# Performance work log

Hardware: AMD Instinct MI355X
Metric: run time of the kernel (lower is better)

The kernel has to match this reference:

```python
import jax, jax.numpy as jnp
import numpy as np

# permutations for num_sources == 3 (matches task2perm[3])
PERMS3 = np.array([[0, 1, 2], [0, 2, 1], [1, 0, 2], [1, 2, 0], [2, 0, 1], [2, 1, 0]])
NUM_SOURCES = 3


def setup_inputs() -> dict:
    key = jax.random.key(0)
    k1, k2 = jax.random.split(key)
    shape = (16, 4096, NUM_SOURCES, 512)  # [bs, seq_len, num_sources, input_dim]
    return {
        "predictions": jax.random.normal(k1, shape, dtype=jnp.float32),
        "ground_truths": jax.random.normal(k2, shape, dtype=jnp.float32),
    }


def reference(predictions, ground_truths):
    n = NUM_SOURCES
    # Pairwise Frobenius distances over (seq_len, input_dim):
    # D[b, s_pred, s_gt] = ||preds[b,:,s_pred,:] - gts[b,:,s_gt,:]||_F
    # computed via ||a||^2 + ||b||^2 - 2<a,b> to avoid 6 permuted diff tensors.
    pn = jnp.sum(predictions * predictions, axis=(1, 3))        # [b, n]
    gn = jnp.sum(ground_truths * ground_truths, axis=(1, 3))    # [b, n]
    cross = jnp.einsum('btsd,btrd->bsr', predictions, ground_truths)  # [b, n, n]
    D = jnp.sqrt(jnp.maximum(pn[:, :, None] + gn[:, None, :] - 2.0 * cross, 0.0))

    perms = jnp.asarray(PERMS3)                                 # [P, n]
    # dists[b, p, s] = D[b, s, perms[p, s]]
    dists = D[:, jnp.arange(n)[None, :], perms]                 # [b, P, n]
    sum_ = jnp.sum(dists, axis=-1) / n                          # [b, P]
    # torch: sqrt(sum_**2).mean() == mean(|sum_|) over batch
    loss_per_perm = jnp.mean(jnp.abs(sum_), axis=0)             # [P]
    return jnp.log(jnp.min(loss_per_perm))
```

## Files before the change

### kernel.cpp

```cpp
#include <hip/hip_runtime.h>
#include <math.h>

#define B_DIM 16
#define T_DIM 4096
#define NSRC 3
#define D_DIM 512
#define DC_PER_ROW (D_DIM / 4)
#define BLOCKS_PER_B 128
#define T_PER_BLOCK (T_DIM / BLOCKS_PER_B)

__device__ __forceinline__ float dot4(float4 a, float4 b) {
    float r = a.x * b.x;
    r = fmaf(a.y, b.y, r);
    r = fmaf(a.z, b.z, r);
    r = fmaf(a.w, b.w, r);
    return r;
}

__global__ __launch_bounds__(256) void minloss_partial(
        const float* __restrict__ P, const float* __restrict__ G,
        float* __restrict__ ws) {
    const int bid   = blockIdx.x;
    const int b     = bid >> 7;
    const int chunk = bid & (BLOCKS_PER_B - 1);
    const int tid   = threadIdx.x;
    const int dc    = tid & (DC_PER_ROW - 1);
    const int tp    = tid >> 7;

    const size_t b_off = (size_t)b * T_DIM * NSRC * DC_PER_ROW;
    const float4* __restrict__ Pb = (const float4*)P + b_off;
    const float4* __restrict__ Gb = (const float4*)G + b_off;

    float acc[15];
#pragma unroll
    for (int k = 0; k < 15; ++k) acc[k] = 0.0f;

    const int t0 = chunk * T_PER_BLOCK;
    for (int t = t0 + tp; t < t0 + T_PER_BLOCK; t += 2) {
        const float4* __restrict__ Pr = Pb + (size_t)t * NSRC * DC_PER_ROW;
        const float4* __restrict__ Gr = Gb + (size_t)t * NSRC * DC_PER_ROW;
        float4 p0 = Pr[dc];
        float4 p1 = Pr[DC_PER_ROW + dc];
        float4 p2 = Pr[2 * DC_PER_ROW + dc];
        float4 g0 = Gr[dc];
        float4 g1 = Gr[DC_PER_ROW + dc];
        float4 g2 = Gr[2 * DC_PER_ROW + dc];

        acc[0] += dot4(p0, p0);
        acc[1] += dot4(p1, p1);
        acc[2] += dot4(p2, p2);
        acc[3] += dot4(g0, g0);
        acc[4] += dot4(g1, g1);
        acc[5] += dot4(g2, g2);
        acc[6]  += dot4(p0, g0);
        acc[7]  += dot4(p0, g1);
        acc[8]  += dot4(p0, g2);
        acc[9]  += dot4(p1, g0);
        acc[10] += dot4(p1, g1);
        acc[11] += dot4(p1, g2);
        acc[12] += dot4(p2, g0);
        acc[13] += dot4(p2, g1);
        acc[14] += dot4(p2, g2);
    }

#pragma unroll
    for (int k = 0; k < 15; ++k) {
        float v = acc[k];
#pragma unroll
        for (int off = 32; off > 0; off >>= 1)
            v += __shfl_down(v, off);
        acc[k] = v;
    }

    __shared__ float sm[4][15];
    const int wid  = tid >> 6;
    const int lane = tid & 63;
    if (lane == 0) {
#pragma unroll
        for (int k = 0; k < 15; ++k) sm[wid][k] = acc[k];
    }
    __syncthreads();
    if (tid < 15) {
        float v = sm[0][tid] + sm[1][tid] + sm[2][tid] + sm[3][tid];
        atomicAdd(&ws[b * 15 + tid], v);
    }
}

__global__ void minloss_finalize(const float* __restrict__ ws,
                                 float* __restrict__ out) {
    if (threadIdx.x != 0 || blockIdx.x != 0) return;
    const int perms[6][3] = {{0,1,2},{0,2,1},{1,0,2},{1,2,0},{2,0,1},{2,1,0}};
    float accp[6] = {0.f, 0.f, 0.f, 0.f, 0.f, 0.f};
    for (int b = 0; b < B_DIM; ++b) {
        const float* w = ws + b * 15;
        float D[3][3];
#pragma unroll
        for (int s = 0; s < 3; ++s)
#pragma unroll
            for (int r = 0; r < 3; ++r) {
                float v = w[s] + w[3 + r] - 2.0f * w[6 + s * 3 + r];
                D[s][r] = sqrtf(fmaxf(v, 0.0f));
            }
#pragma unroll
        for (int p = 0; p < 6; ++p) {
            float su = (D[0][perms[p][0]] + D[1][perms[p][1]] +
                        D[2][perms[p][2]]) * (1.0f / 3.0f);
            accp[p] += fabsf(su);
        }
    }
    float mn = 3.0e38f;
#pragma unroll
    for (int p = 0; p < 6; ++p) {
        float loss = accp[p] * (1.0f / (float)B_DIM);
        mn = fminf(mn, loss);
    }
    out[0] = logf(mn);
}

extern "C" void kernel_launch(void* const* d_in, const int* in_sizes, int n_in,
                              void* d_out, int out_size, void* d_ws, size_t ws_size,
                              hipStream_t stream) {
    const float* P = (const float*)d_in[0];
    const float* G = (const float*)d_in[1];
    float* out = (float*)d_out;
    float* ws  = (float*)d_ws;

    hipMemsetAsync(ws, 0, B_DIM * 15 * sizeof(float), stream);
    minloss_partial<<<B_DIM * BLOCKS_PER_B, 256, 0, stream>>>(P, G, ws);
    minloss_finalize<<<1, 64, 0, stream>>>(ws, out);
}
```

Before: 159.8 us.

## Unroll rows with nontemporal loads and replace atomics with per-block partials

Each loop iteration now loads two time rows using nontemporal vector loads, increasing loads in flight and hinting the cache to avoid retaining streamed data. The per-batch atomicAdd plus workspace memset is replaced by per-block partial writes that a wider finalize kernel reduces in shared memory. This removes a memset launch and atomic contention but adds a serial 128-element reduction per thread in finalize and changes the floating-point summation order.

```diff
diff --git a/kernel.cpp b/kernel.cpp
--- a/kernel.cpp
+++ b/kernel.cpp
@@ -9,7 +9,9 @@
 #define BLOCKS_PER_B 128
 #define T_PER_BLOCK (T_DIM / BLOCKS_PER_B)
 
-__device__ __forceinline__ float dot4(float4 a, float4 b) {
+typedef float f4 __attribute__((ext_vector_type(4)));
+
+__device__ __forceinline__ float dot4(f4 a, f4 b) {
     float r = a.x * b.x;
     r = fmaf(a.y, b.y, r);
     r = fmaf(a.z, b.z, r);
@@ -28,39 +30,48 @@
     const int tp    = tid >> 7;
 
     const size_t b_off = (size_t)b * T_DIM * NSRC * DC_PER_ROW;
-    const float4* __restrict__ Pb = (const float4*)P + b_off;
-    const float4* __restrict__ Gb = (const float4*)G + b_off;
+    const f4* __restrict__ Pb = (const f4*)P + b_off;
+    const f4* __restrict__ Gb = (const f4*)G + b_off;
 
     float acc[15];
 #pragma unroll
     for (int k = 0; k < 15; ++k) acc[k] = 0.0f;
 
     const int t0 = chunk * T_PER_BLOCK;
-    for (int t = t0 + tp; t < t0 + T_PER_BLOCK; t += 2) {
-        const float4* __restrict__ Pr = Pb + (size_t)t * NSRC * DC_PER_ROW;
-        const float4* __restrict__ Gr = Gb + (size_t)t * NSRC * DC_PER_ROW;
-        float4 p0 = Pr[dc];
-        float4 p1 = Pr[DC_PER_ROW + dc];
-        float4 p2 = Pr[2 * DC_PER_ROW + dc];
-        float4 g0 = Gr[dc];
-        float4 g1 = Gr[DC_PER_ROW + dc];
-        float4 g2 = Gr[2 * DC_PER_ROW + dc];
+    for (int t = t0 + tp; t < t0 + T_PER_BLOCK; t += 4) {
+        const f4* __restrict__ Pr0 = Pb + (size_t)t * NSRC * DC_PER_ROW;
+        const f4* __restrict__ Gr0 = Gb + (size_t)t * NSRC * DC_PER_ROW;
+        const f4* __restrict__ Pr1 = Pr0 + 2 * NSRC * DC_PER_ROW;
+        const f4* __restrict__ Gr1 = Gr0 + 2 * NSRC * DC_PER_ROW;
 
-        acc[0] += dot4(p0, p0);
-        acc[1] += dot4(p1, p1);
-        acc[2] += dot4(p2, p2);
-        acc[3] += dot4(g0, g0);
-        acc[4] += dot4(g1, g1);
-        acc[5] += dot4(g2, g2);
-        acc[6]  += dot4(p0, g0);
-        acc[7]  += dot4(p0, g1);
-        acc[8]  += dot4(p0, g2);
-        acc[9]  += dot4(p1, g0);
-        acc[10] += dot4(p1, g1);
-        acc[11] += dot4(p1, g2);
-        acc[12] += dot4(p2, g0);
-        acc[13] += dot4(p2, g1);
-        acc[14] += dot4(p2, g2);
+        f4 p0 = __builtin_nontemporal_load(Pr0 + dc);
+        f4 p1 = __builtin_nontemporal_load(Pr0 + DC_PER_ROW + dc);
+        f4 p2 = __builtin_nontemporal_load(Pr0 + 2 * DC_PER_ROW + dc);
+        f4 g0 = __builtin_nontemporal_load(Gr0 + dc);
+        f4 g1 = __builtin_nontemporal_load(Gr0 + DC_PER_ROW + dc);
+        f4 g2 = __builtin_nontemporal_load(Gr0 + 2 * DC_PER_ROW + dc);
+        f4 q0 = __builtin_nontemporal_load(Pr1 + dc);
+        f4 q1 = __builtin_nontemporal_load(Pr1 + DC_PER_ROW + dc);
+        f4 q2 = __builtin_nontemporal_load(Pr1 + 2 * DC_PER_ROW + dc);
+        f4 h0 = __builtin_nontemporal_load(Gr1 + dc);
+        f4 h1 = __builtin_nontemporal_load(Gr1 + DC_PER_ROW + dc);
+        f4 h2 = __builtin_nontemporal_load(Gr1 + 2 * DC_PER_ROW + dc);
+
+        acc[0] += dot4(p0, p0) + dot4(q0, q0);
+        acc[1] += dot4(p1, p1) + dot4(q1, q1);
+        acc[2] += dot4(p2, p2) + dot4(q2, q2);
+        acc[3] += dot4(g0, g0) + dot4(h0, h0);
+        acc[4] += dot4(g1, g1) + dot4(h1, h1);
+        acc[5] += dot4(g2, g2) + dot4(h2, h2);
+        acc[6]  += dot4(p0, g0) + dot4(q0, h0);
+        acc[7]  += dot4(p0, g1) + dot4(q0, h1);
+        acc[8]  += dot4(p0, g2) + dot4(q0, h2);
+        acc[9]  += dot4(p1, g0) + dot4(q1, h0);
+        acc[10] += dot4(p1, g1) + dot4(q1, h1);
+        acc[11] += dot4(p1, g2) + dot4(q1, h2);
+        acc[12] += dot4(p2, g0) + dot4(q2, h0);
+        acc[13] += dot4(p2, g1) + dot4(q2, h1);
+        acc[14] += dot4(p2, g2) + dot4(q2, h2);
     }
 
 #pragma unroll
@@ -81,40 +92,51 @@
     }
     __syncthreads();
     if (tid < 15) {
-        float v = sm[0][tid] + sm[1][tid] + sm[2][tid] + sm[3][tid];
-        atomicAdd(&ws[b * 15 + tid], v);
+        ws[bid * 15 + tid] = sm[0][tid] + sm[1][tid] + sm[2][tid] + sm[3][tid];
     }
 }
 
 __global__ void minloss_finalize(const float* __restrict__ ws,
                                  float* __restrict__ out) {
-    if (threadIdx.x != 0 || blockIdx.x != 0) return;
-    const int perms[6][3] = {{0,1,2},{0,2,1},{1,0,2},{1,2,0},{2,0,1},{2,1,0}};
-    float accp[6] = {0.f, 0.f, 0.f, 0.f, 0.f, 0.f};
-    for (int b = 0; b < B_DIM; ++b) {
-        const float* w = ws + b * 15;
-        float D[3][3];
+    __shared__ float sm[B_DIM][15];
+    const int tid = threadIdx.x;
+    if (tid < B_DIM * 15) {
+        const int b = tid / 15;
+        const int k = tid % 15;
+        float v = 0.0f;
+        for (int c = 0; c < BLOCKS_PER_B; ++c)
+            v += ws[(b * BLOCKS_PER_B + c) * 15 + k];
+        sm[b][k] = v;
+    }
+    __syncthreads();
+    if (tid == 0) {
+        const int perms[6][3] = {{0,1,2},{0,2,1},{1,0,2},{1,2,0},{2,0,1},{2,1,0}};
+        float accp[6] = {0.f, 0.f, 0.f, 0.f, 0.f, 0.f};
+        for (int b = 0; b < B_DIM; ++b) {
+            const float* w = sm[b];
+            float D[3][3];
 #pragma unroll
-        for (int s = 0; s < 3; ++s)
+            for (int s = 0; s < 3; ++s)
 #pragma unroll
-            for (int r = 0; r < 3; ++r) {
-                float v = w[s] + w[3 + r] - 2.0f * w[6 + s * 3 + r];
-                D[s][r] = sqrtf(fmaxf(v, 0.0f));
+                for (int r = 0; r < 3; ++r) {
+                    float v = w[s] + w[3 + r] - 2.0f * w[6 + s * 3 + r];
+                    D[s][r] = sqrtf(fmaxf(v, 0.0f));
+                }
+#pragma unroll
+            for (int p = 0; p < 6; ++p) {
+                float su = (D[0][perms[p][0]] + D[1][perms[p][1]] +
+                            D[2][perms[p][2]]) * (1.0f / 3.0f);
+                accp[p] += fabsf(su);
             }
+        }
+        float mn = 3.0e38f;
 #pragma unroll
         for (int p = 0; p < 6; ++p) {
-            float su = (D[0][perms[p][0]] + D[1][perms[p][1]] +
-                        D[2][perms[p][2]]) * (1.0f / 3.0f);
-            accp[p] += fabsf(su);
+            float loss = accp[p] * (1.0f / (float)B_DIM);
+            mn = fminf(mn, loss);
         }
+        out[0] = logf(mn);
     }
-    float mn = 3.0e38f;
-#pragma unroll
-    for (int p = 0; p < 6; ++p) {
-        float loss = accp[p] * (1.0f / (float)B_DIM);
-        mn = fminf(mn, loss);
-    }
-    out[0] = logf(mn);
 }
 
 extern "C" void kernel_launch(void* const* d_in, const int* in_sizes, int n_in,
@@ -125,7 +147,6 @@
     float* out = (float*)d_out;
     float* ws  = (float*)d_ws;
 
-    hipMemsetAsync(ws, 0, B_DIM * 15 * sizeof(float), stream);
     minloss_partial<<<B_DIM * BLOCKS_PER_B, 256, 0, stream>>>(P, G, ws);
-    minloss_finalize<<<1, 64, 0, stream>>>(ws, out);
+    minloss_finalize<<<1, 256, 0, stream>>>(ws, out);
 }
```

Measured after the change: 133.6 us. 16.4% less time.
